# Kernel tuning notes

Hardware: AMD Instinct MI355X
Metric: run time of the kernel (lower is better)

## Reference

```python
import jax, jax.numpy as jnp
import numpy as np
from jax import lax

EPS = 1e-5

def layernorm_c(x, w, b):
    # WithBias LayerNorm over channel dim per spatial location (Restormer style)
    mu = jnp.mean(x, axis=1, keepdims=True)
    var = jnp.var(x, axis=1, keepdims=True)  # population variance (unbiased=False)
    xn = (x - mu) / jnp.sqrt(var + EPS)
    return xn * w[None, :, None, None] + b[None, :, None, None]

def conv1x1(x, w, b):
    # w: (C_out, C_in)
    y = jnp.einsum('bchw,oc->bohw', x, w)
    return y + b[None, :, None, None]

def dwconv3x3(x, w, b):
    # w: (C, 1, 3, 3), depthwise
    y = lax.conv_general_dilated(x, w, window_strides=(1, 1), padding=((1, 1), (1, 1)),
                                 dimension_numbers=('NCHW', 'OIHW', 'NCHW'),
                                 feature_group_count=x.shape[1])
    return y + b[None, :, None, None]

def to_patches(x, p):
    B, C, H, W = x.shape
    x = x.reshape(B, C, H // p, p, W // p, p)
    return x.transpose(0, 1, 2, 4, 3, 5)  # (B,C,h,w,p,p)

def from_patches(x):
    B, C, h, w, p1, p2 = x.shape
    return x.transpose(0, 1, 2, 4, 3, 5).reshape(B, C, h * p1, w * p2)

def setup_inputs() -> dict:
    key = jax.random.key(0)
    ks = jax.random.split(key, 12)
    B, C, H, W = 8, 128, 192, 192
    s = 0.05
    return {
        'x': jax.random.normal(ks[0], (B, C, H, W), jnp.float32),
        'evt': jax.random.normal(ks[1], (B, C, H, W), jnp.float32),
        'ln_img_w': jnp.ones((C,), jnp.float32),
        'ln_img_b': jnp.zeros((C,), jnp.float32),
        'ln_evt_w': jnp.ones((C,), jnp.float32),
        'ln_evt_b': jnp.zeros((C,), jnp.float32),
        'q_w': jax.random.normal(ks[2], (2 * C, C), jnp.float32) * s,
        'q_b': jnp.zeros((2 * C,), jnp.float32),
        'q_dw_w': jax.random.normal(ks[3], (2 * C, 1, 3, 3), jnp.float32) * s,
        'q_dw_b': jnp.zeros((2 * C,), jnp.float32),
        'kv_w': jax.random.normal(ks[4], (4 * C, C), jnp.float32) * s,
        'kv_b': jnp.zeros((4 * C,), jnp.float32),
        'kv_dw_w': jax.random.normal(ks[5], (4 * C, 1, 3, 3), jnp.float32) * s,
        'kv_dw_b': jnp.zeros((4 * C,), jnp.float32),
        'ln_corr_w': jnp.ones((2 * C,), jnp.float32),
        'ln_corr_b': jnp.zeros((2 * C,), jnp.float32),
        'proj_w': jax.random.normal(ks[6], (C, 2 * C), jnp.float32) * s,
        'proj_b': jnp.zeros((C,), jnp.float32),
    }

def reference(x, evt, ln_img_w, ln_img_b, ln_evt_w, ln_evt_b,
              q_w, q_b, q_dw_w, q_dw_b, kv_w, kv_b, kv_dw_w, kv_dw_b,
              ln_corr_w, ln_corr_b, proj_w, proj_b):
    p = 8
    C = x.shape[1]
    xn = layernorm_c(x, ln_img_w, ln_img_b)
    en = layernorm_c(evt, ln_evt_w, ln_evt_b)
    q = dwconv3x3(conv1x1(xn, q_w, q_b), q_dw_w, q_dw_b)          # (B,2C,H,W)
    kv = dwconv3x3(conv1x1(en, kv_w, kv_b), kv_dw_w, kv_dw_b)      # (B,4C,H,W)
    k, v = kv[:, :2 * C], kv[:, 2 * C:]
    q_p = to_patches(q, p)  # (B,2C,h,w,p,p)
    k_p = to_patches(k, p)
    corr = jnp.fft.irfft2(jnp.fft.rfft2(q_p.astype(jnp.float32)) *
                          jnp.fft.rfft2(k_p.astype(jnp.float32)), s=(p, p))
    corr = from_patches(corr)                                      # (B,2C,H,W)
    corr = layernorm_c(corr, ln_corr_w, ln_corr_b)
    return conv1x1(v * corr, proj_w, proj_b)
```

## Files before the change

kernel.cpp:

```cpp
#include <hip/hip_runtime.h>
#include <stdint.h>

#define BATCH 8
#define CIN   128
#define HH    192
#define WW    192
#define HW    (HH*WW)
#define PXB   576
#define CH    2

typedef _Float16 half_t;
typedef _Float16 f16x8 __attribute__((ext_vector_type(8)));
typedef _Float16 f16x4 __attribute__((ext_vector_type(4)));
typedef _Float16 f16x2 __attribute__((ext_vector_type(2)));
typedef float    f32x4 __attribute__((ext_vector_type(4)));
typedef float    f32x16 __attribute__((ext_vector_type(16)));
typedef unsigned int u32;

__device__ __forceinline__ float DOT2(u32 a, u32 b, float c) {
#if __has_builtin(__builtin_amdgcn_fdot2)
    return __builtin_amdgcn_fdot2(__builtin_bit_cast(f16x2, a),
                                  __builtin_bit_cast(f16x2, b), c, false);
#else
    f16x2 av = __builtin_bit_cast(f16x2, a), bv = __builtin_bit_cast(f16x2, b);
    return c + (float)av[0] * (float)bv[0] + (float)av[1] * (float)bv[1];
#endif
}

#define SMEM_BYTES 52736
#define WSH_OFF    17408
#define MU_OFF     52224

__global__ __launch_bounds__(256)
void wcvt_kernel(const float* __restrict__ qw, const float* __restrict__ kvw,
                 const float* __restrict__ pw, const float* __restrict__ qdw,
                 const float* __restrict__ kvdw, half_t* __restrict__ out)
{
    int q = blockIdx.x * 256 + threadIdx.x;
    if (q >= 34496) return;
    int idx = q * 4;
    const float* src;
    int off;
    if (idx < 32768)       { src = qw;   off = idx; }
    else if (idx < 98304)  { src = kvw;  off = idx - 32768; }
    else if (idx < 131072) { src = pw;   off = idx - 98304; }
    else if (idx < 133376) { src = qdw;  off = idx - 131072; }
    else                   { src = kvdw; off = idx - 133376; }
    float4 v = *(const float4*)&src[off];
    f16x4 o = { (half_t)v.x, (half_t)v.y, (half_t)v.z, (half_t)v.w };
    *(f16x4*)&out[idx] = o;
}

template<int OC>
__global__ __launch_bounds__(256)
void ln_gemm_kernel(const float* __restrict__ x,
                    const float* __restrict__ lnw, const float* __restrict__ lnb,
                    const half_t* __restrict__ wf16, const float* __restrict__ wb,
                    half_t* __restrict__ out)
{
    __shared__ __attribute__((aligned(16))) char smem[SMEM_BYTES];
    half_t (*As)[136]  = (half_t(*)[136])smem;
    half_t (*Wsh)[136] = (half_t(*)[136])(smem + WSH_OFF);
    float  (*Cst)[68]  = (float (*)[68]) (smem + WSH_OFF);
    float* redA = (float*)(smem + WSH_OFF);
    float* redB = (float*)(smem + WSH_OFF + 1024);
    float* mu_s = (float*)(smem + MU_OFF);
    float* rs_s = mu_s + 64;

    const int tid  = threadIdx.x;
    const int px   = tid & 63;
    const int g    = tid >> 6;
    const int l    = tid & 63;
    const int w    = tid >> 6;
    const int lrow = l & 31;
    const int lk   = (l >> 5) * 8;

    const long p0  = (long)blockIdx.x * 64;
    const int  b   = (int)(p0 / HW);
    const int  hw0 = (int)(p0 - (long)b * HW);

    const float* xb = x + (size_t)b * CIN * HW + hw0 + px;
    float vals[32];
    float s1 = 0.f, s2 = 0.f;
#pragma unroll
    for (int j = 0; j < 32; ++j) {
        float v = xb[(size_t)(g * 32 + j) * HW];
        vals[j] = v; s1 += v; s2 += v * v;
    }
    redA[g * 64 + px] = s1; redB[g * 64 + px] = s2;
    __syncthreads();
    if (tid < 64) {
        float su = redA[tid] + redA[64 + tid] + redA[128 + tid] + redA[192 + tid];
        float sq = redB[tid] + redB[64 + tid] + redB[128 + tid] + redB[192 + tid];
        float mu  = su * (1.f / 128.f);
        float var = sq * (1.f / 128.f) - mu * mu;
        mu_s[tid] = mu;
        rs_s[tid] = rsqrtf(var + 1e-5f);
    }
    __syncthreads();
    {
        float mu = mu_s[px], rs = rs_s[px];
#pragma unroll
        for (int m = 0; m < 4; ++m) {
            f16x8 o;
#pragma unroll
            for (int j = 0; j < 8; ++j) {
                int c = g * 32 + m * 8 + j;
                o[j] = (half_t)((vals[m * 8 + j] - mu) * rs * lnw[c] + lnb[c]);
            }
            *(f16x8*)&As[px][g * 32 + m * 8] = o;
        }
    }

    for (int nc = 0; nc < OC / 128; ++nc) {
        const int n0 = nc * 128;
        if (nc) __syncthreads();
#pragma unroll
        for (int i = 0; i < 8; ++i) {
            int f  = i * 256 + tid;
            int n  = f >> 4;
            int xh = (f & 15) * 8;
            *(f16x8*)&Wsh[n][xh] = *(const f16x8*)&wf16[(size_t)(n0 + n) * CIN + xh];
        }
        __syncthreads();

        f16x8 af[8];
#pragma unroll
        for (int kk = 0; kk < 8; ++kk)
            af[kk] = *(const f16x8*)&Wsh[w * 32 + lrow][kk * 16 + lk];

        f32x16 acc0, acc1;
#pragma unroll
        for (int i = 0; i < 16; ++i) { acc0[i] = 0.f; acc1[i] = 0.f; }
#pragma unroll
        for (int kk = 0; kk < 8; ++kk) {
            f16x8 b0 = *(const f16x8*)&As[lrow][kk * 16 + lk];
            f16x8 b1 = *(const f16x8*)&As[32 + lrow][kk * 16 + lk];
            acc0 = __builtin_amdgcn_mfma_f32_32x32x16_f16(af[kk], b0, acc0, 0, 0, 0);
            acc1 = __builtin_amdgcn_mfma_f32_32x32x16_f16(af[kk], b1, acc1, 0, 0, 0);
        }
        __syncthreads();

#pragma unroll
        for (int r = 0; r < 16; ++r) {
            int oc = w * 32 + (r & 3) + 8 * (r >> 2) + 4 * (l >> 5);
            Cst[oc][lrow]      = acc0[r];
            Cst[oc][32 + lrow] = acc1[r];
        }
        __syncthreads();

#pragma unroll
        for (int i = 0; i < 4; ++i) {
            int idx = i * 256 + tid;
            int oc  = idx >> 3;
            int pxg = idx & 7;
            const float4 a = *(const float4*)&Cst[oc][pxg * 8];
            const float4 c = *(const float4*)&Cst[oc][pxg * 8 + 4];
            float bias = wb[n0 + oc];
            f16x8 o = { (half_t)(a.x + bias), (half_t)(a.y + bias),
                        (half_t)(a.z + bias), (half_t)(a.w + bias),
                        (half_t)(c.x + bias), (half_t)(c.y + bias),
                        (half_t)(c.z + bias), (half_t)(c.w + bias) };
            *(f16x8*)&out[((size_t)b * OC + n0 + oc) * HW + hw0 + pxg * 8] = o;
        }
    }
}

__global__ __launch_bounds__(256)
void corr_strip_kernel(const half_t* __restrict__ q1, const half_t* __restrict__ kv1,
                       const half_t* __restrict__ qdw16, const float* __restrict__ qb,
                       const half_t* __restrict__ kdw16, const float* __restrict__ kb,
                       half_t* __restrict__ corr, half_t* __restrict__ vd)
{
    __shared__ __attribute__((aligned(16))) half_t raw[6][10][208];
    __shared__ __attribute__((aligned(16))) half_t qd[2][8][192];
    __shared__ __attribute__((aligned(16))) half_t krev[2][8][200];

    const int bid = blockIdx.x;
    const int cg  = bid & 127;
    const int ph  = (bid >> 7) % 24;
    const int lb  = (bid >> 7) / 24;
    const int c0  = cg * CH;
    const int tid = threadIdx.x;

    if (tid < 120) {
        int side = tid & 1;
        int row  = (tid >> 1) % 10;
        int a    = tid / 20;
        f16x8 z = {};
        *(f16x8*)&raw[a][row][side ? 200 : 0] = z;
    }

    for (int i = 0; i < 6; ++i) {
        int idx = tid + 256 * i;
        if (idx >= 1440) break;
        int vec = idx % 24;
        int row = (idx / 24) % 10;
        int a   = idx / 240;
        int ch  = a & 1;
        int gh  = ph * 8 - 1 + row;
        f16x8 v = {};
        if (gh >= 0 && gh < HH) {
            const half_t* src;
            if (a < 2)      src = q1  + ((size_t)lb * 256 + c0 + ch) * HW;
            else if (a < 4) src = kv1 + ((size_t)lb * 512 + c0 + ch) * HW;
            else            src = kv1 + ((size_t)lb * 512 + 256 + c0 + ch) * HW;
            v = *(const f16x8*)&src[(size_t)gh * WW + vec * 8];
        }
        *(f16x8*)&raw[a][row][8 + vec * 8] = v;
    }
    __syncthreads();

    for (int i = 0; i < 3; ++i) {
        int unit = tid + 256 * i;
        if (unit >= 576) break;
        int xg2 = unit % 12;
        int u   = (unit / 12) % 8;
        int a   = unit / 96;
        int ch  = a & 1;
        const half_t (*rw)[208] = raw[a];
        const half_t* wt;
        float bias;
        if (a < 2)      { wt = qdw16 + (size_t)(c0 + ch) * 9;       bias = qb[c0 + ch]; }
        else if (a < 4) { wt = kdw16 + (size_t)(c0 + ch) * 9;       bias = kb[c0 + ch]; }
        else            { wt = kdw16 + (size_t)(256 + c0 + ch) * 9; bias = kb[256 + c0 + ch]; }
        u32 w01[3], w2z[3];
#pragma unroll
        for (int dy = 0; dy < 3; ++dy) {
            u32 a0 = (u32)__builtin_bit_cast(unsigned short, wt[dy * 3 + 0]);
            u32 a1 = (u32)__builtin_bit_cast(unsigned short, wt[dy * 3 + 1]);
            u32 a2 = (u32)__builtin_bit_cast(unsigned short, wt[dy * 3 + 2]);
            w01[dy] = a0 | (a1 << 16);
            w2z[dy] = a2;
        }
        const int x0 = xg2 * 16;
        float acc[16];
#pragma unroll
        for (int xx = 0; xx < 16; ++xx) acc[xx] = bias;
#pragma unroll
        for (int dy = 0; dy < 3; ++dy) {
            const half_t* rowp = &rw[u + dy][x0];
            uint4 c0v = *(const uint4*)(rowp);
            uint4 c1v = *(const uint4*)(rowp + 8);
            uint4 c2v = *(const uint4*)(rowp + 16);
            uint4 c3v = *(const uint4*)(rowp + 24);
            u32 H0 = c0v.x, H1 = c0v.y, H2 = c0v.z, H3 = c0v.w;
            u32 H4 = c1v.x, H5 = c1v.y, H6 = c1v.z, H7 = c1v.w;
            u32 H8 = c2v.x, H9 = c2v.y, H10 = c2v.z, H11 = c2v.w;
            u32 H12 = c3v.x;
            u32 H[13] = {H0,H1,H2,H3,H4,H5,H6,H7,H8,H9,H10,H11,H12};
            u32 A[12];
#pragma unroll
            for (int m = 3; m < 12; ++m) A[m] = (H[m] >> 16) | (H[m + 1] << 16);
#pragma unroll
            for (int xx = 0; xx < 16; ++xx) {
                u32 p01 = (xx & 1) ? H[(7 + xx) >> 1] : A[3 + (xx >> 1)];
                u32 p2  = (xx & 1) ? H[(9 + xx) >> 1] : A[4 + (xx >> 1)];
                acc[xx] = DOT2(p01, w01[dy], acc[xx]);
                acc[xx] = DOT2(p2,  w2z[dy], acc[xx]);
            }
        }
        f16x8 o0, o1;
#pragma unroll
        for (int xx = 0; xx < 8; ++xx) { o0[xx] = (half_t)acc[xx]; o1[xx] = (half_t)acc[8 + xx]; }
        if (a < 2) {
            *(f16x8*)&qd[ch][u][x0]     = o0;
            *(f16x8*)&qd[ch][u][x0 + 8] = o1;
        } else if (a < 4) {
            f16x8 r0v, r1v;
            r0v[0] = (half_t)acc[0];
            r1v[0] = (half_t)acc[8];
#pragma unroll
            for (int j = 1; j < 8; ++j) {
                r0v[j] = (half_t)acc[8 - j];
                r1v[j] = (half_t)acc[16 - j];
            }
            *(f16x8*)&krev[ch][u][x0]     = r0v;
            *(f16x8*)&krev[ch][u][x0 + 8] = r1v;
        } else {
            half_t* dst = &vd[((size_t)lb * 256 + c0 + ch) * HW + (size_t)(ph * 8 + u) * WW + x0];
            *(f16x8*)dst       = o0;
            *(f16x8*)(dst + 8) = o1;
        }
    }
    __syncthreads();

    for (int i = 0; i < 2; ++i) {
        int unit = tid + 256 * i;
        if (unit >= 384) break;
        int c   = unit / 192;
        int rem = unit % 192;
        int pw  = rem >> 3;
        int u   = rem & 7;
        float acc[8];
#pragma unroll
        for (int v = 0; v < 8; ++v) acc[v] = 0.f;
#pragma unroll
        for (int s = 0; s < 8; ++s) {
            int r = (u - s) & 7;
            uint4 q4 = *(const uint4*)&qd[c][s][pw * 8];
            uint4 k4 = *(const uint4*)&krev[c][r][pw * 8];
            u32 Q[4] = {q4.x, q4.y, q4.z, q4.w};
            u32 K[4] = {k4.x, k4.y, k4.z, k4.w};
            u32 S[4];
#pragma unroll
            for (int m = 0; m < 4; ++m) S[m] = (K[m] >> 16) | (K[(m + 1) & 3] << 16);
#pragma unroll
            for (int v = 0; v < 8; ++v) {
                const int o = 8 - v;
#pragma unroll
                for (int tt = 0; tt < 4; ++tt) {
                    u32 pr = (o & 1) ? S[(((o - 1) >> 1) + tt) & 3]
                                     : K[((o >> 1) + tt) & 3];
                    acc[v] = DOT2(Q[tt], pr, acc[v]);
                }
            }
        }
        f16x8 ov;
#pragma unroll
        for (int v = 0; v < 8; ++v) ov[v] = (half_t)acc[v];
        *(f16x8*)&corr[((size_t)lb * 256 + c0 + c) * HW + (size_t)(ph * 8 + u) * WW + pw * 8] = ov;
    }
}

__global__ __launch_bounds__(256)
void proj_kernel(const half_t* __restrict__ corr, const half_t* __restrict__ vd,
                 const float* __restrict__ lnw, const float* __restrict__ lnb,
                 const half_t* __restrict__ wp16, const float* __restrict__ wb,
                 float* __restrict__ out)
{
    __shared__ __attribute__((aligned(16))) char smem[SMEM_BYTES];
    half_t (*As)[136]  = (half_t(*)[136])smem;
    half_t (*Wsh)[136] = (half_t(*)[136])(smem + WSH_OFF);
    float  (*Cst)[68]  = (float (*)[68]) (smem + WSH_OFF);
    float* redA = (float*)(smem + WSH_OFF);
    float* redB = (float*)(smem + WSH_OFF + 1024);
    float* mu_s = (float*)(smem + MU_OFF);
    float* rs_s = mu_s + 64;

    const int tid  = threadIdx.x;
    const int px   = tid & 63;
    const int g    = tid >> 6;
    const int l    = tid & 63;
    const int w    = tid >> 6;
    const int lrow = l & 31;
    const int lk   = (l >> 5) * 8;

    const long p0  = (long)blockIdx.x * 64;
    const int  lb  = (int)(p0 / HW);
    const int  hw0 = (int)(p0 - (long)lb * HW);

    const half_t* cb = corr + (size_t)lb * 256 * HW + hw0 + px;
    const half_t* vb = vd   + (size_t)lb * 256 * HW + hw0 + px;

    float s1 = 0.f, s2 = 0.f;
#pragma unroll 8
    for (int j = 0; j < 64; ++j) {
        float cv = (float)cb[(size_t)(g * 64 + j) * HW];
        s1 += cv; s2 += cv * cv;
    }
    redA[g * 64 + px] = s1; redB[g * 64 + px] = s2;
    __syncthreads();
    if (tid < 64) {
        float su = redA[tid] + redA[64 + tid] + redA[128 + tid] + redA[192 + tid];
        float sq = redB[tid] + redB[64 + tid] + redB[128 + tid] + redB[192 + tid];
        float mu  = su * (1.f / 256.f);
        float var = sq * (1.f / 256.f) - mu * mu;
        mu_s[tid] = mu;
        rs_s[tid] = rsqrtf(var + 1e-5f);
    }
    __syncthreads();
    const float mu = mu_s[px], rs = rs_s[px];

    f32x16 acc0, acc1;
#pragma unroll
    for (int i = 0; i < 16; ++i) { acc0[i] = 0.f; acc1[i] = 0.f; }

    for (int kc = 0; kc < 2; ++kc) {
        if (kc) __syncthreads();
#pragma unroll
        for (int m = 0; m < 4; ++m) {
            f16x8 o;
#pragma unroll
            for (int j = 0; j < 8; ++j) {
                int c = kc * 128 + g * 32 + m * 8 + j;
                float cv = (float)cb[(size_t)c * HW];
                float vv = (float)vb[(size_t)c * HW];
                o[j] = (half_t)(((cv - mu) * rs * lnw[c] + lnb[c]) * vv);
            }
            *(f16x8*)&As[px][g * 32 + m * 8] = o;
        }
#pragma unroll
        for (int i = 0; i < 8; ++i) {
            int f  = i * 256 + tid;
            int n  = f >> 4;
            int xh = (f & 15) * 8;
            *(f16x8*)&Wsh[n][xh] = *(const f16x8*)&wp16[(size_t)n * 256 + kc * 128 + xh];
        }
        __syncthreads();

        f16x8 af[8];
#pragma unroll
        for (int kk = 0; kk < 8; ++kk)
            af[kk] = *(const f16x8*)&Wsh[w * 32 + lrow][kk * 16 + lk];
#pragma unroll
        for (int kk = 0; kk < 8; ++kk) {
            f16x8 b0 = *(const f16x8*)&As[lrow][kk * 16 + lk];
            f16x8 b1 = *(const f16x8*)&As[32 + lrow][kk * 16 + lk];
            acc0 = __builtin_amdgcn_mfma_f32_32x32x16_f16(af[kk], b0, acc0, 0, 0, 0);
            acc1 = __builtin_amdgcn_mfma_f32_32x32x16_f16(af[kk], b1, acc1, 0, 0, 0);
        }
    }
    __syncthreads();

#pragma unroll
    for (int r = 0; r < 16; ++r) {
        int oc = w * 32 + (r & 3) + 8 * (r >> 2) + 4 * (l >> 5);
        Cst[oc][lrow]      = acc0[r];
        Cst[oc][32 + lrow] = acc1[r];
    }
    __syncthreads();

#pragma unroll
    for (int i = 0; i < 8; ++i) {
        int idx = i * 256 + tid;
        int oc  = idx >> 4;
        int pxq = idx & 15;
        float4 a = *(const float4*)&Cst[oc][pxq * 4];
        float bias = wb[oc];
        a.x += bias; a.y += bias; a.z += bias; a.w += bias;
        *(float4*)&out[((size_t)lb * 128 + oc) * HW + hw0 + pxq * 4] = a;
    }
}

extern "C" void kernel_launch(void* const* d_in, const int* in_sizes, int n_in,
                              void* d_out, int out_size, void* d_ws, size_t ws_size,
                              hipStream_t stream)
{
    const float* x        = (const float*)d_in[0];
    const float* evt      = (const float*)d_in[1];
    const float* ln_img_w = (const float*)d_in[2];
    const float* ln_img_b = (const float*)d_in[3];
    const float* ln_evt_w = (const float*)d_in[4];
    const float* ln_evt_b = (const float*)d_in[5];
    const float* q_w      = (const float*)d_in[6];
    const float* q_b      = (const float*)d_in[7];
    const float* q_dw_w   = (const float*)d_in[8];
    const float* q_dw_b   = (const float*)d_in[9];
    const float* kv_w     = (const float*)d_in[10];
    const float* kv_b     = (const float*)d_in[11];
    const float* kv_dw_w  = (const float*)d_in[12];
    const float* kv_dw_b  = (const float*)d_in[13];
    const float* ln_corr_w= (const float*)d_in[14];
    const float* ln_corr_b= (const float*)d_in[15];
    const float* proj_w   = (const float*)d_in[16];
    const float* proj_b   = (const float*)d_in[17];
    float* out = (float*)d_out;

    const size_t wtail = (ws_size - 278528) & ~(size_t)255;
    half_t* wf    = (half_t*)((char*)d_ws + wtail);
    half_t* wq16  = wf;
    half_t* wkv16 = wf + 32768;
    half_t* wp16  = wf + 98304;
    half_t* qdw16 = wf + 131072;
    half_t* kdw16 = wf + 133376;

    const size_t per_b = (size_t)(256 + 512 + 256 + 256) * HW * sizeof(half_t);
    int PB = 1;
    if      (wtail >= 8 * per_b) PB = 8;
    else if (wtail >= 4 * per_b) PB = 4;
    else if (wtail >= 2 * per_b) PB = 2;

    half_t* q1   = (half_t*)d_ws;
    half_t* kv1  = q1  + (size_t)PB * 256 * HW;
    half_t* vd   = kv1 + (size_t)PB * 512 * HW;
    half_t* corr = vd  + (size_t)PB * 256 * HW;

    dim3 blk(256);
    wcvt_kernel<<<135, blk, 0, stream>>>(q_w, kv_w, proj_w, q_dw_w, kv_dw_w, wf);

    for (int b0 = 0; b0 < BATCH; b0 += PB) {
        int nb = PB;
        ln_gemm_kernel<256><<<nb * PXB, blk, 0, stream>>>(
            x + (size_t)b0 * CIN * HW, ln_img_w, ln_img_b, wq16, q_b, q1);
        ln_gemm_kernel<512><<<nb * PXB, blk, 0, stream>>>(
            evt + (size_t)b0 * CIN * HW, ln_evt_w, ln_evt_b, wkv16, kv_b, kv1);
        corr_strip_kernel<<<nb * 24 * 128, blk, 0, stream>>>(
            q1, kv1, qdw16, q_dw_b, kdw16, kv_dw_b, corr, vd);
        proj_kernel<<<nb * PXB, blk, 0, stream>>>(
            corr, vd, ln_corr_w, ln_corr_b, wp16, proj_b,
            out + (size_t)b0 * 128 * HW);
    }
}
```

Before: 733.1 us.

## Load GEMM weight fragments directly from global, drop weight LDS staging

Measured after the change: 779.5 us. 6.3% more time.

```diff
diff --git a/kernel.cpp b/kernel.cpp
--- a/kernel.cpp
+++ b/kernel.cpp
@@ -8,6 +8,7 @@
 #define HW    (HH*WW)
 #define PXB   576
 #define CH    2
+#define RS    216
 
 typedef _Float16 half_t;
 typedef _Float16 f16x8 __attribute__((ext_vector_type(8)));
@@ -27,9 +28,7 @@
 #endif
 }
 
-#define SMEM_BYTES 52736
-#define WSH_OFF    17408
-#define MU_OFF     52224
+#define GSMEM 34816
 
 __global__ __launch_bounds__(256)
 void wcvt_kernel(const float* __restrict__ qw, const float* __restrict__ kvw,
@@ -58,14 +57,13 @@
                     const half_t* __restrict__ wf16, const float* __restrict__ wb,
                     half_t* __restrict__ out)
 {
-    __shared__ __attribute__((aligned(16))) char smem[SMEM_BYTES];
+    __shared__ __attribute__((aligned(16))) char smem[GSMEM];
     half_t (*As)[136]  = (half_t(*)[136])smem;
-    half_t (*Wsh)[136] = (half_t(*)[136])(smem + WSH_OFF);
-    float  (*Cst)[68]  = (float (*)[68]) (smem + WSH_OFF);
-    float* redA = (float*)(smem + WSH_OFF);
-    float* redB = (float*)(smem + WSH_OFF + 1024);
-    float* mu_s = (float*)(smem + MU_OFF);
-    float* rs_s = mu_s + 64;
+    float  (*Cst)[68]  = (float (*)[68])smem;
+    float* redA = (float*)(smem + 17408);
+    float* redB = (float*)(smem + 18432);
+    float* mu_s = (float*)(smem + 19456);
+    float* rs_s = (float*)(smem + 19712);
 
     const int tid  = threadIdx.x;
     const int px   = tid & 63;
@@ -111,33 +109,35 @@
             *(f16x8*)&As[px][g * 32 + m * 8] = o;
         }
     }
+    __syncthreads();
+
+    f16x8 bf0[8], bf1[8];
+#pragma unroll
+    for (int kk = 0; kk < 8; ++kk) {
+        bf0[kk] = *(const f16x8*)&As[lrow][kk * 16 + lk];
+        bf1[kk] = *(const f16x8*)&As[32 + lrow][kk * 16 + lk];
+    }
 
     for (int nc = 0; nc < OC / 128; ++nc) {
         const int n0 = nc * 128;
-        if (nc) __syncthreads();
-#pragma unroll
-        for (int i = 0; i < 8; ++i) {
-            int f  = i * 256 + tid;
-            int n  = f >> 4;
-            int xh = (f & 15) * 8;
-            *(f16x8*)&Wsh[n][xh] = *(const f16x8*)&wf16[(size_t)(n0 + n) * CIN + xh];
-        }
-        __syncthreads();
-
         f16x8 af[8];
+        const half_t* wr = wf16 + (size_t)(n0 + w * 32 + lrow) * CIN + lk;
 #pragma unroll
         for (int kk = 0; kk < 8; ++kk)
-            af[kk] = *(const f16x8*)&Wsh[w * 32 + lrow][kk * 16 + lk];
-
+            af[kk] = *(const f16x8*)&wr[kk * 16];
         f32x16 acc0, acc1;
 #pragma unroll
-        for (int i = 0; i < 16; ++i) { acc0[i] = 0.f; acc1[i] = 0.f; }
+        for (int q4 = 0; q4 < 4; ++q4) {
+            float4 bv = *(const float4*)&wb[n0 + w * 32 + 8 * q4 + 4 * (l >> 5)];
+            acc0[q4 * 4 + 0] = bv.x; acc0[q4 * 4 + 1] = bv.y;
+            acc0[q4 * 4 + 2] = bv.z; acc0[q4 * 4 + 3] = bv.w;
+            acc1[q4 * 4 + 0] = bv.x; acc1[q4 * 4 + 1] = bv.y;
+            acc1[q4 * 4 + 2] = bv.z; acc1[q4 * 4 + 3] = bv.w;
+        }
 #pragma unroll
         for (int kk = 0; kk < 8; ++kk) {
-            f16x8 b0 = *(const f16x8*)&As[lrow][kk * 16 + lk];
-            f16x8 b1 = *(const f16x8*)&As[32 + lrow][kk * 16 + lk];
-            acc0 = __builtin_amdgcn_mfma_f32_32x32x16_f16(af[kk], b0, acc0, 0, 0, 0);
-            acc1 = __builtin_amdgcn_mfma_f32_32x32x16_f16(af[kk], b1, acc1, 0, 0, 0);
+            acc0 = __builtin_amdgcn_mfma_f32_32x32x16_f16(af[kk], bf0[kk], acc0, 0, 0, 0);
+            acc1 = __builtin_amdgcn_mfma_f32_32x32x16_f16(af[kk], bf1[kk], acc1, 0, 0, 0);
         }
         __syncthreads();
 
@@ -156,11 +156,8 @@
             int pxg = idx & 7;
             const float4 a = *(const float4*)&Cst[oc][pxg * 8];
             const float4 c = *(const float4*)&Cst[oc][pxg * 8 + 4];
-            float bias = wb[n0 + oc];
-            f16x8 o = { (half_t)(a.x + bias), (half_t)(a.y + bias),
-                        (half_t)(a.z + bias), (half_t)(a.w + bias),
-                        (half_t)(c.x + bias), (half_t)(c.y + bias),
-                        (half_t)(c.z + bias), (half_t)(c.w + bias) };
+            f16x8 o = { (half_t)a.x, (half_t)a.y, (half_t)a.z, (half_t)a.w,
+                        (half_t)c.x, (half_t)c.y, (half_t)c.z, (half_t)c.w };
             *(f16x8*)&out[((size_t)b * OC + n0 + oc) * HW + hw0 + pxg * 8] = o;
         }
     }
@@ -172,9 +169,9 @@
                        const half_t* __restrict__ kdw16, const float* __restrict__ kb,
                        half_t* __restrict__ corr, half_t* __restrict__ vd)
 {
-    __shared__ __attribute__((aligned(16))) half_t raw[6][10][208];
-    __shared__ __attribute__((aligned(16))) half_t qd[2][8][192];
-    __shared__ __attribute__((aligned(16))) half_t krev[2][8][200];
+    __shared__ __attribute__((aligned(16))) half_t raw[6][10][RS];
+    __shared__ __attribute__((aligned(16))) half_t qd[2][8][RS];
+    __shared__ __attribute__((aligned(16))) half_t krev[2][8][RS];
 
     const int bid = blockIdx.x;
     const int cg  = bid & 127;
@@ -214,11 +211,11 @@
     for (int i = 0; i < 3; ++i) {
         int unit = tid + 256 * i;
         if (unit >= 576) break;
-        int xg2 = unit % 12;
-        int u   = (unit / 12) % 8;
+        int u   = unit & 7;
+        int xg2 = (unit >> 3) % 12;
         int a   = unit / 96;
         int ch  = a & 1;
-        const half_t (*rw)[208] = raw[a];
+        const half_t (*rw)[RS] = raw[a];
         const half_t* wt;
         float bias;
         if (a < 2)      { wt = qdw16 + (size_t)(c0 + ch) * 9;       bias = qb[c0 + ch]; }
@@ -244,11 +241,8 @@
             uint4 c1v = *(const uint4*)(rowp + 8);
             uint4 c2v = *(const uint4*)(rowp + 16);
             uint4 c3v = *(const uint4*)(rowp + 24);
-            u32 H0 = c0v.x, H1 = c0v.y, H2 = c0v.z, H3 = c0v.w;
-            u32 H4 = c1v.x, H5 = c1v.y, H6 = c1v.z, H7 = c1v.w;
-            u32 H8 = c2v.x, H9 = c2v.y, H10 = c2v.z, H11 = c2v.w;
-            u32 H12 = c3v.x;
-            u32 H[13] = {H0,H1,H2,H3,H4,H5,H6,H7,H8,H9,H10,H11,H12};
+            u32 H[13] = {c0v.x,c0v.y,c0v.z,c0v.w, c1v.x,c1v.y,c1v.z,c1v.w,
+                         c2v.x,c2v.y,c2v.z,c2v.w, c3v.x};
             u32 A[12];
 #pragma unroll
             for (int m = 3; m < 12; ++m) A[m] = (H[m] >> 16) | (H[m + 1] << 16);
@@ -329,14 +323,13 @@
                  const half_t* __restrict__ wp16, const float* __restrict__ wb,
                  float* __restrict__ out)
 {
-    __shared__ __attribute__((aligned(16))) char smem[SMEM_BYTES];
+    __shared__ __attribute__((aligned(16))) char smem[GSMEM];
     half_t (*As)[136]  = (half_t(*)[136])smem;
-    half_t (*Wsh)[136] = (half_t(*)[136])(smem + WSH_OFF);
-    float  (*Cst)[68]  = (float (*)[68]) (smem + WSH_OFF);
-    float* redA = (float*)(smem + WSH_OFF);
-    float* redB = (float*)(smem + WSH_OFF + 1024);
-    float* mu_s = (float*)(smem + MU_OFF);
-    float* rs_s = mu_s + 64;
+    float  (*Cst)[68]  = (float (*)[68])smem;
+    float* redA = (float*)(smem + 17408);
+    float* redB = (float*)(smem + 18432);
+    float* mu_s = (float*)(smem + 19456);
+    float* rs_s = (float*)(smem + 19712);
 
     const int tid  = threadIdx.x;
     const int px   = tid & 63;
@@ -374,7 +367,13 @@
 
     f32x16 acc0, acc1;
 #pragma unroll
-    for (int i = 0; i < 16; ++i) { acc0[i] = 0.f; acc1[i] = 0.f; }
+    for (int q4 = 0; q4 < 4; ++q4) {
+        float4 bv = *(const float4*)&wb[w * 32 + 8 * q4 + 4 * (l >> 5)];
+        acc0[q4 * 4 + 0] = bv.x; acc0[q4 * 4 + 1] = bv.y;
+        acc0[q4 * 4 + 2] = bv.z; acc0[q4 * 4 + 3] = bv.w;
+        acc1[q4 * 4 + 0] = bv.x; acc1[q4 * 4 + 1] = bv.y;
+        acc1[q4 * 4 + 2] = bv.z; acc1[q4 * 4 + 3] = bv.w;
+    }
 
     for (int kc = 0; kc < 2; ++kc) {
         if (kc) __syncthreads();
@@ -390,25 +389,20 @@
             }
             *(f16x8*)&As[px][g * 32 + m * 8] = o;
         }
-#pragma unroll
-        for (int i = 0; i < 8; ++i) {
-            int f  = i * 256 + tid;
-            int n  = f >> 4;
-            int xh = (f & 15) * 8;
-            *(f16x8*)&Wsh[n][xh] = *(const f16x8*)&wp16[(size_t)n * 256 + kc * 128 + xh];
-        }
         __syncthreads();
 
-        f16x8 af[8];
-#pragma unroll
-        for (int kk = 0; kk < 8; ++kk)
-            af[kk] = *(const f16x8*)&Wsh[w * 32 + lrow][kk * 16 + lk];
+        f16x8 bf0[8], bf1[8];
 #pragma unroll
         for (int kk = 0; kk < 8; ++kk) {
-            f16x8 b0 = *(const f16x8*)&As[lrow][kk * 16 + lk];
-            f16x8 b1 = *(const f16x8*)&As[32 + lrow][kk * 16 + lk];
-            acc0 = __builtin_amdgcn_mfma_f32_32x32x16_f16(af[kk], b0, acc0, 0, 0, 0);
-            acc1 = __builtin_amdgcn_mfma_f32_32x32x16_f16(af[kk], b1, acc1, 0, 0, 0);
+            bf0[kk] = *(const f16x8*)&As[lrow][kk * 16 + lk];
+            bf1[kk] = *(const f16x8*)&As[32 + lrow][kk * 16 + lk];
+        }
+        const half_t* wr = wp16 + (size_t)(w * 32 + lrow) * 256 + kc * 128 + lk;
+#pragma unroll
+        for (int kk = 0; kk < 8; ++kk) {
+            f16x8 af = *(const f16x8*)&wr[kk * 16];
+            acc0 = __builtin_amdgcn_mfma_f32_32x32x16_f16(af, bf0[kk], acc0, 0, 0, 0);
+            acc1 = __builtin_amdgcn_mfma_f32_32x32x16_f16(af, bf1[kk], acc1, 0, 0, 0);
         }
     }
     __syncthreads();
@@ -427,8 +421,6 @@
         int oc  = idx >> 4;
         int pxq = idx & 15;
         float4 a = *(const float4*)&Cst[oc][pxq * 4];
-        float bias = wb[oc];
-        a.x += bias; a.y += bias; a.z += bias; a.w += bias;
         *(float4*)&out[((size_t)lb * 128 + oc) * HW + hw0 + pxq * 4] = a;
     }
 }
```
